# Optimization experiments

Measured on AMD Instinct MI355X. Metric: run time of the kernel, lower is better.

## Reference

```python
import jax, jax.numpy as jnp
import numpy as np

N = 100000        # nodes
E = 1600000       # edges (before self-loops)
F_IN = 128        # input feature dim
HID = 32          # hidden_channels
HEADS = 2
HC = HID * HEADS  # 64, per-conv output width (concat=True)
OUT = 40          # out_channels
NEG_SLOPE = 0.2   # PyG GATConv leaky_relu slope
BN_EPS = 1e-5


def setup_inputs() -> dict:
    key = jax.random.key(0)
    ks = jax.random.split(key, 16)
    g = lambda k, shape, s: jax.random.normal(k, shape, jnp.float32) * s
    node_feat = jax.random.normal(ks[0], (N, F_IN), jnp.float32)
    edge_index = jax.random.randint(ks[1], (2, E), 0, N, jnp.int32)
    inp = {
        "node_feat": node_feat,
        "edge_index": edge_index,
        "W1": g(ks[2], (F_IN, HC), 1.0 / np.sqrt(F_IN)),
        "a_src1": g(ks[3], (HEADS, HID), 0.1),
        "a_dst1": g(ks[4], (HEADS, HID), 0.1),
        "b1": jnp.zeros((HC,), jnp.float32),
        # BatchNorm1d(64) in eval mode (running stats)
        "bn_gamma": jnp.ones((HC,), jnp.float32),
        "bn_beta": jnp.zeros((HC,), jnp.float32),
        "bn_mean": g(ks[5], (HC,), 0.1),
        "bn_var": jax.random.uniform(ks[6], (HC,), jnp.float32, 0.5, 1.5),
        "W2": g(ks[7], (HC, HC), 1.0 / np.sqrt(HC)),
        "a_src2": g(ks[8], (HEADS, HID), 0.1),
        "a_dst2": g(ks[9], (HEADS, HID), 0.1),
        "b2": jnp.zeros((HC,), jnp.float32),
        # final projection 64 -> 40
        "Wf": g(ks[10], (HC, OUT), 1.0 / np.sqrt(HC)),
        "bf": jnp.zeros((OUT,), jnp.float32),
    }
    return inp


def _gat_layer(x, src, dst, W, a_s, a_d, b):
    # x: [N, Fin] -> h: [N, H, C]
    h = (x @ W).reshape(N, HEADS, HID)
    alpha_src = jnp.einsum('nhc,hc->nh', h, a_s)   # [N, H]
    alpha_dst = jnp.einsum('nhc,hc->nh', h, a_d)   # [N, H]
    e = jax.nn.leaky_relu(alpha_src[src] + alpha_dst[dst], NEG_SLOPE)  # [Etot, H]
    m = jax.lax.stop_gradient(jax.ops.segment_max(e, dst, num_segments=N))
    ex = jnp.exp(e - m[dst])
    denom = jax.ops.segment_sum(ex, dst, num_segments=N)
    alpha = ex / (denom[dst] + 1e-16)              # softmax over incoming edges
    msg = h[src] * alpha[:, :, None]               # [Etot, H, C]
    out = jax.ops.segment_sum(msg, dst, num_segments=N)  # [N, H, C]
    return out.reshape(N, HC) + b


def reference(node_feat, edge_index, W1, a_src1, a_dst1, b1,
              bn_gamma, bn_beta, bn_mean, bn_var,
              W2, a_src2, a_dst2, b2, Wf, bf):
    # add self-loops (PyG GATConv default add_self_loops=True)
    loop = jnp.arange(N, dtype=edge_index.dtype)
    src = jnp.concatenate([edge_index[0], loop])
    dst = jnp.concatenate([edge_index[1], loop])

    x1 = _gat_layer(node_feat, src, dst, W1, a_src1, a_dst1, b1)
    # BatchNorm1d eval + ELU (dropout is identity in eval)
    x1 = (x1 - bn_mean) * (bn_gamma / jnp.sqrt(bn_var + BN_EPS)) + bn_beta
    x1 = jax.nn.elu(x1)

    x2 = _gat_layer(x1, src, dst, W2, a_src2, a_dst2, b2)

    # JumpingKnowledge 'max': elementwise max over layer outputs
    xj = jnp.maximum(x1, x2)
    return xj @ Wf + bf
```

## Files before the change

kernel.cpp:

```cpp
#include <hip/hip_runtime.h>
#include <hip/hip_bf16.h>

#define N_NODES 100000
#define E_EDGES 1600000
#define ETOT    1700000
#define NB_SCAN 391
#define EQ4     400000
#define NB_EQ4  1563
#define EQ8     200000
#define NB_EQ8  782
#define NGB     1563
#define F_IN    128
#define HC      64
#define OUT_C   40
#define NEG_SLOPE 0.2f
#define BN_EPS  1e-5f

#define P_W1   0
#define P_AS1  8192
#define P_AD1  8256
#define P_B1   8320
#define P_BNG  8384
#define P_BNB  8448
#define P_BNM  8512
#define P_BNV  8576
#define P_W2   8640
#define P_AS2  12736
#define P_AD2  12800
#define P_B2   12864
#define P_WF   12928
#define P_BF   15488
#define P_TOT  15528

typedef __attribute__((ext_vector_type(8))) short short8;
typedef __attribute__((ext_vector_type(4))) float floatx4;
typedef __attribute__((ext_vector_type(4))) unsigned int uintx4;

__device__ __forceinline__ unsigned short f2bf(float f) {
    unsigned int u = __float_as_uint(f);
    unsigned int r = u + 0x7FFFu + ((u >> 16) & 1u);
    return (unsigned short)(r >> 16);
}

__device__ __forceinline__ float leaky(float v) { return v > 0.f ? v : NEG_SLOPE * v; }

__device__ __forceinline__ float red64(float v) {
#pragma unroll
    for (int off = 32; off > 0; off >>= 1) v += __shfl_xor(v, off, 64);
    return v;
}
__device__ __forceinline__ float red16(float v) {
#pragma unroll
    for (int off = 8; off > 0; off >>= 1) v += __shfl_xor(v, off, 64);
    return v;
}

__global__ __launch_bounds__(64) void detect_kernel(const unsigned short* __restrict__ x,
                                                    int* __restrict__ flag) {
    int t = threadIdx.x;
    bool huge = false;
#pragma unroll
    for (int i = 0; i < 4; ++i) {
        unsigned short u = x[(t * 4 + i) * 2];
        float v = __uint_as_float(((unsigned int)u) << 16);
        if (!(fabsf(v) < 1e4f)) huge = true;
    }
    unsigned long long b = __ballot(huge);
    if (t == 0) *flag = (b != 0ull) ? 1 : 0;
}

struct CvtArgs { const void* ptr[14]; int len[14]; };

__global__ __launch_bounds__(256) void cvt_params_kernel(CvtArgs a,
                                                         const int* __restrict__ flag,
                                                         float* __restrict__ dst) {
    int f = *flag;
    int i = blockIdx.x * 256 + threadIdx.x;
    if (i >= P_TOT) return;
    int k = 0, off = 0;
    while (i >= off + a.len[k]) { off += a.len[k]; ++k; }
    int j = i - off;
    float v = f ? ((const float*)a.ptr[k])[j]
                : __bfloat162float(((const __hip_bfloat16*)a.ptr[k])[j]);
    dst[i] = v;
}

__global__ __launch_bounds__(256) void build_frags_kernel(const float* __restrict__ prm,
                                                          unsigned short* __restrict__ fw1,
                                                          unsigned short* __restrict__ fw2) {
    int i = blockIdx.x * 256 + threadIdx.x;
    if (i < 8192) {
        int j = i & 7, l = (i >> 3) & 63, q = (i >> 9) & 3, t = i >> 11;
        int k = q * 32 + (l >> 4) * 8 + j;
        int n = t * 16 + (l & 15);
        fw1[i] = f2bf(prm[P_W1 + k * 64 + n]);
    } else if (i < 12288) {
        int f = i - 8192;
        int j = f & 7, l = (f >> 3) & 63, q = (f >> 9) & 1, t = f >> 10;
        int k = q * 32 + (l >> 4) * 8 + j;
        int n = t * 16 + (l & 15);
        fw2[f] = f2bf(prm[P_W2 + k * 64 + n]);
    }
}

__global__ __launch_bounds__(256) void fused_hist_gemm1_kernel(
        const int* __restrict__ ei, int* __restrict__ deg, int4* __restrict__ rank4,
        const void* __restrict__ x, const unsigned short* __restrict__ fw1,
        const float* __restrict__ prm, const int* __restrict__ flag,
        unsigned short* __restrict__ h_bf, float* __restrict__ as_,
        float* __restrict__ ad_) {
    __shared__ short lx[4 * 4 * 64 * 8];
    if (blockIdx.x < NB_EQ8) {
        int i8 = blockIdx.x * 256 + threadIdx.x;
        if (i8 >= EQ8) return;
        const unsigned long long* dst2 = (const unsigned long long*)(ei + E_EDGES);
        unsigned long long p0 = __builtin_nontemporal_load(&dst2[i8 * 4]);
        unsigned long long p1 = __builtin_nontemporal_load(&dst2[i8 * 4 + 1]);
        unsigned long long p2 = __builtin_nontemporal_load(&dst2[i8 * 4 + 2]);
        unsigned long long p3 = __builtin_nontemporal_load(&dst2[i8 * 4 + 3]);
        int d0 = (int)(p0 & 0xFFFFFFFFull), d1 = (int)(p0 >> 32);
        int d2 = (int)(p1 & 0xFFFFFFFFull), d3 = (int)(p1 >> 32);
        int d4 = (int)(p2 & 0xFFFFFFFFull), d5 = (int)(p2 >> 32);
        int d6 = (int)(p3 & 0xFFFFFFFFull), d7 = (int)(p3 >> 32);
        int r0 = atomicAdd(&deg[d0], 1);
        int r1 = atomicAdd(&deg[d1], 1);
        int r2 = atomicAdd(&deg[d2], 1);
        int r3 = atomicAdd(&deg[d3], 1);
        int r4 = atomicAdd(&deg[d4], 1);
        int r5 = atomicAdd(&deg[d5], 1);
        int r6 = atomicAdd(&deg[d6], 1);
        int r7 = atomicAdd(&deg[d7], 1);
        rank4[i8 * 2]     = make_int4(r0, r1, r2, r3);
        rank4[i8 * 2 + 1] = make_int4(r4, r5, r6, r7);
        return;
    }

    int t = threadIdx.x;
    int f = *flag;
    int base = (blockIdx.x - NB_EQ8) * 64;

#pragma unroll
    for (int i = 0; i < 4; ++i) {
        int cid = i * 256 + t;
        int m = cid >> 4, c = cid & 15;
        int q = c >> 2, g = c & 3;
        int loff = (((m >> 4) * 4 + q) * 64 + g * 16 + (m & 15)) * 8;
        int srow = base + m; if (srow > N_NODES - 1) srow = N_NODES - 1;
        short8 s;
        if (f) {
            const float4* p = (const float4*)((const float*)x + ((size_t)srow << 7) + (c << 3));
            float4 u0 = p[0], u1 = p[1];
            s[0] = (short)f2bf(u0.x); s[1] = (short)f2bf(u0.y);
            s[2] = (short)f2bf(u0.z); s[3] = (short)f2bf(u0.w);
            s[4] = (short)f2bf(u1.x); s[5] = (short)f2bf(u1.y);
            s[6] = (short)f2bf(u1.z); s[7] = (short)f2bf(u1.w);
        } else {
            s = *(const short8*)((const unsigned short*)x + ((size_t)srow << 7) + (c << 3));
        }
        *(short8*)&lx[loff] = s;
    }
    __syncthreads();

    int w = t >> 6, lane = t & 63;
    short8 a[4];
#pragma unroll
    for (int q = 0; q < 4; ++q) a[q] = *(short8*)&lx[((w * 4 + q) * 64 + lane) * 8];

    const short8* bw = (const short8*)fw1;
    floatx4 acc[4];
#pragma unroll
    for (int tt = 0; tt < 4; ++tt) acc[tt] = (floatx4){0.f, 0.f, 0.f, 0.f};
#pragma unroll
    for (int tt = 0; tt < 4; ++tt) {
#pragma unroll
        for (int q = 0; q < 4; ++q) {
            short8 b = bw[(tt * 4 + q) * 64 + lane];
            acc[tt] = __builtin_amdgcn_mfma_f32_16x16x32_bf16(a[q], b, acc[tt], 0, 0, 0);
        }
    }

    int cl = lane & 15, grp = lane >> 4;
#pragma unroll
    for (int tt = 0; tt < 4; ++tt) {
#pragma unroll
        for (int r = 0; r < 4; ++r) {
            int node = base + w * 16 + grp * 4 + r;
            if (node < N_NODES)
                h_bf[(size_t)node * 64 + tt * 16 + cl] = f2bf(acc[tt][r]);
        }
    }

    float as0 = prm[P_AS1 + 0  + cl], as1 = prm[P_AS1 + 16 + cl],
          as2 = prm[P_AS1 + 32 + cl], as3 = prm[P_AS1 + 48 + cl];
    float ad0 = prm[P_AD1 + 0  + cl], ad1 = prm[P_AD1 + 16 + cl],
          ad2 = prm[P_AD1 + 32 + cl], ad3 = prm[P_AD1 + 48 + cl];
#pragma unroll
    for (int r = 0; r < 4; ++r) {
        float sh0 = red16(acc[0][r] * as0 + acc[1][r] * as1);
        float sh1 = red16(acc[2][r] * as2 + acc[3][r] * as3);
        float dh0 = red16(acc[0][r] * ad0 + acc[1][r] * ad1);
        float dh1 = red16(acc[2][r] * ad2 + acc[3][r] * ad3);
        int node = base + w * 16 + grp * 4 + r;
        if (cl == 0 && node < N_NODES) {
            as_[node * 2] = sh0;  as_[node * 2 + 1] = sh1;
            ad_[node * 2] = dh0;  ad_[node * 2 + 1] = dh1;
        }
    }
}

__global__ __launch_bounds__(256) void scanA_kernel(const int* __restrict__ deg,
                                                    int* __restrict__ bsum) {
    __shared__ int sm[256];
    int t = threadIdx.x;
    int i = blockIdx.x * 256 + t;
    sm[t] = (i < N_NODES) ? deg[i] + 1 : 0;
    __syncthreads();
    for (int off = 128; off > 0; off >>= 1) {
        if (t < off) sm[t] += sm[t + off];
        __syncthreads();
    }
    if (t == 0) bsum[blockIdx.x] = sm[0];
}

__global__ __launch_bounds__(512) void scanB_kernel(const int* __restrict__ bsum,
                                                    int* __restrict__ boff,
                                                    int* __restrict__ row_start) {
    __shared__ int sm[512];
    int t = threadIdx.x;
    int v = (t < NB_SCAN) ? bsum[t] : 0;
    sm[t] = v;
    __syncthreads();
    for (int off = 1; off < 512; off <<= 1) {
        int o = (t >= off) ? sm[t - off] : 0;
        __syncthreads();
        sm[t] += o;
        __syncthreads();
    }
    if (t < NB_SCAN) boff[t] = sm[t] - v;
    if (t == NB_SCAN - 1) row_start[N_NODES] = sm[t];
}

__global__ __launch_bounds__(256) void scanC_kernel(const int* __restrict__ deg,
                                                    const int* __restrict__ boff,
                                                    int* __restrict__ row_start,
                                                    int* __restrict__ col) {
    __shared__ int sm[256];
    int t = threadIdx.x;
    int i = blockIdx.x * 256 + t;
    int v = (i < N_NODES) ? deg[i] + 1 : 0;
    sm[t] = v;
    __syncthreads();
    for (int off = 1; off < 256; off <<= 1) {
        int o = (t >= off) ? sm[t - off] : 0;
        __syncthreads();
        sm[t] += o;
        __syncthreads();
    }
    if (i < N_NODES) {
        int excl = sm[t] - v + boff[blockIdx.x];
        row_start[i] = excl;
        col[excl]    = i;
    }
}

__global__ __launch_bounds__(256) void scatter_kernel(const int* __restrict__ ei,
                                                      const int4* __restrict__ rank4,
                                                      const int* __restrict__ row_start,
                                                      int* __restrict__ col) {
    int i4 = blockIdx.x * 256 + threadIdx.x;
    if (i4 >= EQ4) return;
    const unsigned long long* dst2 = (const unsigned long long*)(ei + E_EDGES);
    const unsigned long long* src2 = (const unsigned long long*)ei;
    unsigned long long p0 = __builtin_nontemporal_load(&dst2[i4 * 2]);
    unsigned long long p1 = __builtin_nontemporal_load(&dst2[i4 * 2 + 1]);
    unsigned long long q0 = __builtin_nontemporal_load(&src2[i4 * 2]);
    unsigned long long q1 = __builtin_nontemporal_load(&src2[i4 * 2 + 1]);
    int4 r = rank4[i4];
    int d0 = (int)(p0 & 0xFFFFFFFFull), d1 = (int)(p0 >> 32);
    int d2 = (int)(p1 & 0xFFFFFFFFull), d3 = (int)(p1 >> 32);
    int s0 = (int)(q0 & 0xFFFFFFFFull), s1 = (int)(q0 >> 32);
    int s2 = (int)(q1 & 0xFFFFFFFFull), s3 = (int)(q1 >> 32);
    int b0 = row_start[d0];
    int b1 = row_start[d1];
    int b2 = row_start[d2];
    int b3 = row_start[d3];
    col[b0 + 1 + r.x] = s0;
    col[b1 + 1 + r.y] = s1;
    col[b2 + 1 + r.z] = s2;
    col[b3 + 1 + r.w] = s3;
}

__global__ __launch_bounds__(128) void gemm2_kernel(const unsigned short* __restrict__ x1_bf,
                                                    const unsigned short* __restrict__ fw2,
                                                    const float* __restrict__ prm,
                                                    unsigned short* __restrict__ h_bf,
                                                    float* __restrict__ as_,
                                                    float* __restrict__ ad_) {
    __shared__ short lx[2 * 2 * 64 * 8];
    int t = threadIdx.x;
    int base = blockIdx.x * 32;

#pragma unroll
    for (int i = 0; i < 2; ++i) {
        int cid = i * 128 + t;
        int m = cid >> 3, c = cid & 7;
        int q = c >> 2, g = c & 3;
        int loff = (((m >> 4) * 2 + q) * 64 + g * 16 + (m & 15)) * 8;
        short8 s = *(const short8*)(x1_bf + ((size_t)(base + m) << 6) + (c << 3));
        *(short8*)&lx[loff] = s;
    }
    __syncthreads();

    int w = t >> 6, lane = t & 63;
    short8 a[2];
#pragma unroll
    for (int q = 0; q < 2; ++q) a[q] = *(short8*)&lx[((w * 2 + q) * 64 + lane) * 8];

    const short8* bw = (const short8*)fw2;
    floatx4 acc[4];
#pragma unroll
    for (int tt = 0; tt < 4; ++tt) acc[tt] = (floatx4){0.f, 0.f, 0.f, 0.f};
#pragma unroll
    for (int tt = 0; tt < 4; ++tt) {
#pragma unroll
        for (int q = 0; q < 2; ++q) {
            short8 b = bw[(tt * 2 + q) * 64 + lane];
            acc[tt] = __builtin_amdgcn_mfma_f32_16x16x32_bf16(a[q], b, acc[tt], 0, 0, 0);
        }
    }

    int cl = lane & 15, grp = lane >> 4;
#pragma unroll
    for (int tt = 0; tt < 4; ++tt) {
#pragma unroll
        for (int r = 0; r < 4; ++r) {
            int node = base + w * 16 + grp * 4 + r;
            h_bf[(size_t)node * 64 + tt * 16 + cl] = f2bf(acc[tt][r]);
        }
    }

    float as0 = prm[P_AS2 + 0  + cl], as1 = prm[P_AS2 + 16 + cl],
          as2 = prm[P_AS2 + 32 + cl], as3 = prm[P_AS2 + 48 + cl];
    float ad0 = prm[P_AD2 + 0  + cl], ad1 = prm[P_AD2 + 16 + cl],
          ad2 = prm[P_AD2 + 32 + cl], ad3 = prm[P_AD2 + 48 + cl];
#pragma unroll
    for (int r = 0; r < 4; ++r) {
        float sh0 = red16(acc[0][r] * as0 + acc[1][r] * as1);
        float sh1 = red16(acc[2][r] * as2 + acc[3][r] * as3);
        float dh0 = red16(acc[0][r] * ad0 + acc[1][r] * ad1);
        float dh1 = red16(acc[2][r] * ad2 + acc[3][r] * ad3);
        if (cl == 0) {
            int node = base + w * 16 + grp * 4 + r;
            as_[node * 2] = sh0;  as_[node * 2 + 1] = sh1;
            ad_[node * 2] = dh0;  ad_[node * 2 + 1] = dh1;
        }
    }
}

__device__ __forceinline__ float slot_reduce(float acc[8], int lane) {
    int slot = lane & 7;
    bool b2 = (slot & 4) != 0;
#pragma unroll
    for (int q = 0; q < 4; ++q) {
        float send = b2 ? acc[q] : acc[q + 4];
        float recv = __shfl_xor(send, 4, 64);
        acc[q] = (b2 ? acc[q + 4] : acc[q]) + recv;
    }
    bool b1 = (slot & 2) != 0;
#pragma unroll
    for (int q = 0; q < 2; ++q) {
        float send = b1 ? acc[q] : acc[q + 2];
        float recv = __shfl_xor(send, 2, 64);
        acc[q] = (b1 ? acc[q + 2] : acc[q]) + recv;
    }
    bool b0 = (slot & 1) != 0;
    float send = b0 ? acc[0] : acc[1];
    float recv = __shfl_xor(send, 1, 64);
    return (b0 ? acc[1] : acc[0]) + recv;
}

template<int NK>
__device__ __forceinline__ void agg_rounds(const unsigned short* __restrict__ hb,
                                           const float* __restrict__ as_,
                                           const int* __restrict__ col,
                                           int rs, int koff, int last,
                                           int slot, int hi, float advh,
                                           float acc[8], float& sw) {
    int ce[NK]; float av[NK]; uintx4 dv[NK];
#pragma unroll
    for (int k = 0; k < NK; ++k) {
        int e = rs + koff + k * 8 + slot;
        ce[k] = col[e < last ? e : last];
    }
#pragma unroll
    for (int k = 0; k < NK; ++k)
        dv[k] = *(const uintx4*)(hb + ((size_t)ce[k] << 6));
#pragma unroll
    for (int k = 0; k < NK; ++k)
        av[k] = as_[ce[k] * 2 + hi];

    if constexpr (NK == 1) {
        asm volatile("" : "+v"(dv[0]), "+v"(av[0]));
    } else if constexpr (NK == 2) {
        asm volatile("" : "+v"(dv[0]), "+v"(dv[1]), "+v"(av[0]), "+v"(av[1]));
    } else if constexpr (NK == 3) {
        asm volatile("" : "+v"(dv[0]), "+v"(dv[1]), "+v"(dv[2]),
                          "+v"(av[0]), "+v"(av[1]), "+v"(av[2]));
    } else {
        asm volatile("" : "+v"(dv[0]), "+v"(dv[1]), "+v"(dv[2]), "+v"(dv[3]),
                          "+v"(av[0]), "+v"(av[1]), "+v"(av[2]), "+v"(av[3]));
    }

#pragma unroll
    for (int k = 0; k < NK; ++k) {
        int e = rs + koff + k * 8 + slot;
        float w = (e <= last) ? __expf(leaky(av[k] + advh)) : 0.f;
        sw += w;
#pragma unroll
        for (int q = 0; q < 4; ++q) {
            unsigned int dw = dv[k][q];
            acc[2 * q]     = fmaf(w, __uint_as_float(dw << 16),         acc[2 * q]);
            acc[2 * q + 1] = fmaf(w, __uint_as_float(dw & 0xFFFF0000u), acc[2 * q + 1]);
        }
    }
}

__device__ __forceinline__ float agg_core(const unsigned short* __restrict__ h_bf,
                                          const float* __restrict__ as_,
                                          const float* __restrict__ ad_,
                                          const int* __restrict__ col,
                                          int v, int rs, int re, int lane) {
    int deg  = re - rs;
    int slot = lane & 7;
    int cg   = lane >> 3;
    int hi   = cg >> 2;
    if (deg <= 64) {
        float advh = ad_[v * 2 + hi];
        const unsigned short* hb = h_bf + (cg << 3);
        int last = re - 1;
        float acc[8] = {0.f,0.f,0.f,0.f,0.f,0.f,0.f,0.f};
        float sw = 0.f;

        if (deg <= 8) {
            agg_rounds<1>(hb, as_, col, rs, 0, last, slot, hi, advh, acc, sw);
        } else if (deg <= 16) {
            agg_rounds<2>(hb, as_, col, rs, 0, last, slot, hi, advh, acc, sw);
        } else if (deg <= 24) {
            agg_rounds<3>(hb, as_, col, rs, 0, last, slot, hi, advh, acc, sw);
        } else {
            agg_rounds<4>(hb, as_, col, rs, 0, last, slot, hi, advh, acc, sw);
            if (deg > 32)
                agg_rounds<4>(hb, as_, col, rs, 32, last, slot, hi, advh, acc, sw);
        }

        sw += __shfl_xor(sw, 1, 64);
        sw += __shfl_xor(sw, 2, 64);
        sw += __shfl_xor(sw, 4, 64);
        float rdh = 1.f / (sw + 1e-16f);

        return slot_reduce(acc, lane) * rdh;
    } else {
        int head = lane >> 5;
        float adv0 = ad_[v * 2], adv1 = ad_[v * 2 + 1];
        float advh = head ? adv1 : adv0;
        float s0 = 0.f, s1 = 0.f;
        for (int e = rs + lane; e < re; e += 64) {
            int s = col[e];
            float2 av = *(const float2*)&as_[s * 2];
            s0 += __expf(leaky(av.x + adv0));
            s1 += __expf(leaky(av.y + adv1));
        }
        s0 = red64(s0); s1 = red64(s1);
        float rdh = 1.f / ((head ? s1 : s0) + 1e-16f);
        float a0 = 0.f;
        for (int e = rs; e < re; ++e) {
            int s = col[e];
            float w = __expf(leaky(as_[s * 2 + head] + advh));
            unsigned short u = h_bf[(size_t)s * 64 + lane];
            a0 = fmaf(w, __uint_as_float(((unsigned int)u) << 16), a0);
        }
        return a0 * rdh;
    }
}

__global__ __launch_bounds__(256, 6) void agg1_kernel(const unsigned short* __restrict__ h_bf,
                                                   const float* __restrict__ as_,
                                                   const float* __restrict__ ad_,
                                                   const int* __restrict__ row_start,
                                                   const int* __restrict__ col,
                                                   const float* __restrict__ bias,
                                                   const float* __restrict__ bn_g,
                                                   const float* __restrict__ bn_b,
                                                   const float* __restrict__ bn_m,
                                                   const float* __restrict__ bn_v,
                                                   unsigned short* __restrict__ x1_bf) {
    int t = threadIdx.x, wid = t >> 6, lane = t & 63;
    int v = blockIdx.x * 4 + wid;
    int rs = row_start[v], re = row_start[v + 1];
    float acc = agg_core(h_bf, as_, ad_, col, v, rs, re, lane);
    float r = acc + bias[lane];
    float scale = bn_g[lane] * rsqrtf(bn_v[lane] + BN_EPS);
    r = (r - bn_m[lane]) * scale + bn_b[lane];
    r = r > 0.f ? r : expm1f(r);
    x1_bf[(size_t)v * 64 + lane] = f2bf(r);
}

__global__ __launch_bounds__(256, 6) void agg2_kernel(const unsigned short* __restrict__ h_bf,
                                                   const float* __restrict__ as_,
                                                   const float* __restrict__ ad_,
                                                   const int* __restrict__ row_start,
                                                   const int* __restrict__ col,
                                                   const float* __restrict__ prm,
                                                   const unsigned short* __restrict__ x1_bf,
                                                   const int* __restrict__ flag,
                                                   void* __restrict__ out) {
    __shared__ float Wfs[2560];
    __shared__ float xsh[4][64];
    int t = threadIdx.x;
#pragma unroll
    for (int i = 0; i < 10; ++i) Wfs[i * 256 + t] = prm[P_WF + i * 256 + t];

    int wid = t >> 6, lane = t & 63;
    int v = blockIdx.x * 4 + wid;
    int rs = row_start[v], re = row_start[v + 1];
    float acc = agg_core(h_bf, as_, ad_, col, v, rs, re, lane);
    float x2 = acc + prm[P_B2 + lane];
    unsigned short u = x1_bf[(size_t)v * 64 + lane];
    float x1v = __uint_as_float(((unsigned int)u) << 16);
    xsh[wid][lane] = fmaxf(x1v, x2);
    __syncthreads();

    if (t < 160) {
        int n = t / 40, o = t - n * 40;
        float po = 0.f;
#pragma unroll
        for (int c = 0; c < 64; c += 4) {
            po = fmaf(xsh[n][c],     Wfs[c * 40 + o],       po);
            po = fmaf(xsh[n][c + 1], Wfs[(c + 1) * 40 + o], po);
            po = fmaf(xsh[n][c + 2], Wfs[(c + 2) * 40 + o], po);
            po = fmaf(xsh[n][c + 3], Wfs[(c + 3) * 40 + o], po);
        }
        float r = po + prm[P_BF + o];
        size_t idx = (size_t)(blockIdx.x * 4 + n) * 40 + o;
        if (*flag) ((float*)out)[idx] = r;
        else ((__hip_bfloat16*)out)[idx] = __float2bfloat16(r);
    }
}

extern "C" void kernel_launch(void* const* d_in, const int* in_sizes, int n_in,
                              void* d_out, int out_size, void* d_ws, size_t ws_size,
                              hipStream_t stream) {
    (void)in_sizes; (void)n_in; (void)out_size; (void)ws_size;
    const void* node_feat = d_in[0];
    const int*  edge_idx  = (const int*)d_in[1];

    char* ws = (char*)d_ws;
    size_t off = 0;
    auto alloc = [&](size_t bytes) -> void* {
        void* p = ws + off;
        off += (bytes + 255) & ~(size_t)255;
        return p;
    };
    unsigned short* h_bf  = (unsigned short*)alloc((size_t)N_NODES * 64 * 2);
    unsigned short* x1_bf = (unsigned short*)alloc((size_t)N_NODES * 64 * 2);
    float* as_ = (float*)alloc((size_t)N_NODES * 2 * 4);
    float* ad_ = (float*)alloc((size_t)N_NODES * 2 * 4);
    int* deg       = (int*)alloc((size_t)N_NODES * 4);
    int* row_start = (int*)alloc((size_t)(N_NODES + 1) * 4);
    int4* rank4    = (int4*)alloc((size_t)EQ4 * 16);
    int* col       = (int*)alloc((size_t)ETOT * 4);
    int* bsum      = (int*)alloc((size_t)NB_SCAN * 4);
    int* boff      = (int*)alloc((size_t)NB_SCAN * 4);
    float* prm     = (float*)alloc((size_t)P_TOT * 4);
    unsigned short* fw1 = (unsigned short*)alloc(8192 * 2);
    unsigned short* fw2 = (unsigned short*)alloc(4096 * 2);
    int* flag      = (int*)alloc(256);

    detect_kernel<<<1, 64, 0, stream>>>((const unsigned short*)node_feat, flag);
    CvtArgs ca;
    const int lens[14] = {8192, 64, 64, 64, 64, 64, 64, 64, 4096, 64, 64, 64, 2560, 40};
    for (int i = 0; i < 14; ++i) { ca.ptr[i] = d_in[i + 2]; ca.len[i] = lens[i]; }
    cvt_params_kernel<<<(P_TOT + 255) / 256, 256, 0, stream>>>(ca, flag, prm);
    build_frags_kernel<<<48, 256, 0, stream>>>(prm, fw1, fw2);

    hipMemsetAsync(deg, 0, (size_t)N_NODES * 4, stream);
    fused_hist_gemm1_kernel<<<NB_EQ8 + NGB, 256, 0, stream>>>(
        edge_idx, deg, rank4, node_feat, fw1, prm, flag, h_bf, as_, ad_);
    scanA_kernel<<<NB_SCAN, 256, 0, stream>>>(deg, bsum);
    scanB_kernel<<<1, 512, 0, stream>>>(bsum, boff, row_start);
    scanC_kernel<<<NB_SCAN, 256, 0, stream>>>(deg, boff, row_start, col);
    scatter_kernel<<<NB_EQ4, 256, 0, stream>>>(edge_idx, rank4, row_start, col);

    agg1_kernel<<<N_NODES / 4, 256, 0, stream>>>(h_bf, as_, ad_, row_start, col,
                                                 prm + P_B1, prm + P_BNG, prm + P_BNB,
                                                 prm + P_BNM, prm + P_BNV, x1_bf);
    gemm2_kernel<<<N_NODES / 32, 128, 0, stream>>>(x1_bf, fw2, prm,
                                                   h_bf, as_, ad_);
    agg2_kernel<<<N_NODES / 4, 256, 0, stream>>>(h_bf, as_, ad_, row_start, col,
                                                 prm, x1_bf, flag, d_out);
}
```

Baseline: 367.0 us.

## Build CSR via two-level bucket sort instead of per-node global atomics

Replaces the per-destination global atomic histogram, three-pass scan and rank-based scatter with a bucketed counting sort over 196 buckets of 512 nodes. Block-local LDS histograms reduce global atomics, edges are staged into an intermediate buffer grouped by bucket, and a per-bucket kernel builds row_start and col with LDS atomics and a local scan. This targets the cost of random global atomics and scattered writes, but adds an extra 8-byte-per-edge staging write and read, and the final CSR kernel uses only 196 blocks, so it may leave the GPU underutilized.

```diff
diff --git a/kernel.cpp b/kernel.cpp
--- a/kernel.cpp
+++ b/kernel.cpp
@@ -4,12 +4,10 @@
 #define N_NODES 100000
 #define E_EDGES 1600000
 #define ETOT    1700000
-#define NB_SCAN 391
-#define EQ4     400000
-#define NB_EQ4  1563
 #define EQ8     200000
 #define NB_EQ8  782
 #define NGB     1563
+#define NBUK    196
 #define F_IN    128
 #define HC      64
 #define OUT_C   40
@@ -103,39 +101,45 @@
     }
 }
 
+
 __global__ __launch_bounds__(256) void fused_hist_gemm1_kernel(
-        const int* __restrict__ ei, int* __restrict__ deg, int4* __restrict__ rank4,
+        const int* __restrict__ ei, int* __restrict__ bkt_cnt,
         const void* __restrict__ x, const unsigned short* __restrict__ fw1,
         const float* __restrict__ prm, const int* __restrict__ flag,
         unsigned short* __restrict__ h_bf, float* __restrict__ as_,
         float* __restrict__ ad_) {
     __shared__ short lx[4 * 4 * 64 * 8];
+    int t = threadIdx.x;
     if (blockIdx.x < NB_EQ8) {
-        int i8 = blockIdx.x * 256 + threadIdx.x;
-        if (i8 >= EQ8) return;
-        const unsigned long long* dst2 = (const unsigned long long*)(ei + E_EDGES);
-        unsigned long long p0 = __builtin_nontemporal_load(&dst2[i8 * 4]);
-        unsigned long long p1 = __builtin_nontemporal_load(&dst2[i8 * 4 + 1]);
-        unsigned long long p2 = __builtin_nontemporal_load(&dst2[i8 * 4 + 2]);
-        unsigned long long p3 = __builtin_nontemporal_load(&dst2[i8 * 4 + 3]);
-        int d0 = (int)(p0 & 0xFFFFFFFFull), d1 = (int)(p0 >> 32);
-        int d2 = (int)(p1 & 0xFFFFFFFFull), d3 = (int)(p1 >> 32);
-        int d4 = (int)(p2 & 0xFFFFFFFFull), d5 = (int)(p2 >> 32);
-        int d6 = (int)(p3 & 0xFFFFFFFFull), d7 = (int)(p3 >> 32);
-        int r0 = atomicAdd(&deg[d0], 1);
-        int r1 = atomicAdd(&deg[d1], 1);
-        int r2 = atomicAdd(&deg[d2], 1);
-        int r3 = atomicAdd(&deg[d3], 1);
-        int r4 = atomicAdd(&deg[d4], 1);
-        int r5 = atomicAdd(&deg[d5], 1);
-        int r6 = atomicAdd(&deg[d6], 1);
-        int r7 = atomicAdd(&deg[d7], 1);
-        rank4[i8 * 2]     = make_int4(r0, r1, r2, r3);
-        rank4[i8 * 2 + 1] = make_int4(r4, r5, r6, r7);
+        int* cnt = (int*)lx;
+        if (t < NBUK) cnt[t] = 0;
+        __syncthreads();
+        int i8 = blockIdx.x * 256 + t;
+        if (i8 < EQ8) {
+            const unsigned long long* dst2 = (const unsigned long long*)(ei + E_EDGES);
+            unsigned long long p0 = __builtin_nontemporal_load(&dst2[i8 * 4]);
+            unsigned long long p1 = __builtin_nontemporal_load(&dst2[i8 * 4 + 1]);
+            unsigned long long p2 = __builtin_nontemporal_load(&dst2[i8 * 4 + 2]);
+            unsigned long long p3 = __builtin_nontemporal_load(&dst2[i8 * 4 + 3]);
+            atomicAdd(&cnt[(int)(p0 & 0xFFFFFFFFull) >> 9], 1);
+            atomicAdd(&cnt[(int)(p0 >> 32) >> 9], 1);
+            atomicAdd(&cnt[(int)(p1 & 0xFFFFFFFFull) >> 9], 1);
+            atomicAdd(&cnt[(int)(p1 >> 32) >> 9], 1);
+            atomicAdd(&cnt[(int)(p2 & 0xFFFFFFFFull) >> 9], 1);
+            atomicAdd(&cnt[(int)(p2 >> 32) >> 9], 1);
+            atomicAdd(&cnt[(int)(p3 & 0xFFFFFFFFull) >> 9], 1);
+            atomicAdd(&cnt[(int)(p3 >> 32) >> 9], 1);
+        }
+        __syncthreads();
+        if (t < NBUK) {
+            int tb = t + (int)(blockIdx.x % NBUK);
+            tb -= (tb >= NBUK) ? NBUK : 0;
+            int c = cnt[tb];
+            if (c) atomicAdd(&bkt_cnt[tb], c);
+        }
         return;
     }
 
-    int t = threadIdx.x;
     int f = *flag;
     int base = (blockIdx.x - NB_EQ8) * 64;
 
@@ -208,46 +212,13 @@
     }
 }
 
-__global__ __launch_bounds__(256) void scanA_kernel(const int* __restrict__ deg,
-                                                    int* __restrict__ bsum) {
+__global__ __launch_bounds__(256) void bucket_scan_kernel(const int* __restrict__ bkt_cnt,
+                                                          int* __restrict__ boff,
+                                                          int* __restrict__ bcur,
+                                                          int* __restrict__ row_start) {
     __shared__ int sm[256];
     int t = threadIdx.x;
-    int i = blockIdx.x * 256 + t;
-    sm[t] = (i < N_NODES) ? deg[i] + 1 : 0;
-    __syncthreads();
-    for (int off = 128; off > 0; off >>= 1) {
-        if (t < off) sm[t] += sm[t + off];
-        __syncthreads();
-    }
-    if (t == 0) bsum[blockIdx.x] = sm[0];
-}
-
-__global__ __launch_bounds__(512) void scanB_kernel(const int* __restrict__ bsum,
-                                                    int* __restrict__ boff,
-                                                    int* __restrict__ row_start) {
-    __shared__ int sm[512];
-    int t = threadIdx.x;
-    int v = (t < NB_SCAN) ? bsum[t] : 0;
-    sm[t] = v;
-    __syncthreads();
-    for (int off = 1; off < 512; off <<= 1) {
-        int o = (t >= off) ? sm[t - off] : 0;
-        __syncthreads();
-        sm[t] += o;
-        __syncthreads();
-    }
-    if (t < NB_SCAN) boff[t] = sm[t] - v;
-    if (t == NB_SCAN - 1) row_start[N_NODES] = sm[t];
-}
-
-__global__ __launch_bounds__(256) void scanC_kernel(const int* __restrict__ deg,
-                                                    const int* __restrict__ boff,
-                                                    int* __restrict__ row_start,
-                                                    int* __restrict__ col) {
-    __shared__ int sm[256];
-    int t = threadIdx.x;
-    int i = blockIdx.x * 256 + t;
-    int v = (i < N_NODES) ? deg[i] + 1 : 0;
+    int v = (t < NBUK) ? bkt_cnt[t] : 0;
     sm[t] = v;
     __syncthreads();
     for (int off = 1; off < 256; off <<= 1) {
@@ -256,38 +227,108 @@
         sm[t] += o;
         __syncthreads();
     }
-    if (i < N_NODES) {
-        int excl = sm[t] - v + boff[blockIdx.x];
-        row_start[i] = excl;
-        col[excl]    = i;
-    }
-}
-
-__global__ __launch_bounds__(256) void scatter_kernel(const int* __restrict__ ei,
-                                                      const int4* __restrict__ rank4,
-                                                      const int* __restrict__ row_start,
-                                                      int* __restrict__ col) {
-    int i4 = blockIdx.x * 256 + threadIdx.x;
-    if (i4 >= EQ4) return;
-    const unsigned long long* dst2 = (const unsigned long long*)(ei + E_EDGES);
-    const unsigned long long* src2 = (const unsigned long long*)ei;
-    unsigned long long p0 = __builtin_nontemporal_load(&dst2[i4 * 2]);
-    unsigned long long p1 = __builtin_nontemporal_load(&dst2[i4 * 2 + 1]);
-    unsigned long long q0 = __builtin_nontemporal_load(&src2[i4 * 2]);
-    unsigned long long q1 = __builtin_nontemporal_load(&src2[i4 * 2 + 1]);
-    int4 r = rank4[i4];
-    int d0 = (int)(p0 & 0xFFFFFFFFull), d1 = (int)(p0 >> 32);
-    int d2 = (int)(p1 & 0xFFFFFFFFull), d3 = (int)(p1 >> 32);
-    int s0 = (int)(q0 & 0xFFFFFFFFull), s1 = (int)(q0 >> 32);
-    int s2 = (int)(q1 & 0xFFFFFFFFull), s3 = (int)(q1 >> 32);
-    int b0 = row_start[d0];
-    int b1 = row_start[d1];
-    int b2 = row_start[d2];
-    int b3 = row_start[d3];
-    col[b0 + 1 + r.x] = s0;
-    col[b1 + 1 + r.y] = s1;
-    col[b2 + 1 + r.z] = s2;
-    col[b3 + 1 + r.w] = s3;
+    if (t < NBUK) { int e = sm[t] - v; boff[t] = e; bcur[t] = e; }
+    if (t == NBUK - 1) boff[NBUK] = sm[t];
+    if (t == 0) row_start[N_NODES] = ETOT;
+}
+
+__global__ __launch_bounds__(256) void bucket_scatter_kernel(const int* __restrict__ ei,
+                                                             int* __restrict__ bcur,
+                                                             unsigned long long* __restrict__ estage) {
+    __shared__ int cnt[NBUK];
+    __shared__ int base[NBUK];
+    int t = threadIdx.x;
+    if (t < NBUK) cnt[t] = 0;
+    __syncthreads();
+    int i8 = blockIdx.x * 256 + t;
+    bool valid = i8 < EQ8;
+    int d[8], s[8], rl[8];
+    if (valid) {
+        const unsigned long long* dst2 = (const unsigned long long*)(ei + E_EDGES);
+        const unsigned long long* src2 = (const unsigned long long*)ei;
+        unsigned long long p0 = __builtin_nontemporal_load(&dst2[i8 * 4]);
+        unsigned long long p1 = __builtin_nontemporal_load(&dst2[i8 * 4 + 1]);
+        unsigned long long p2 = __builtin_nontemporal_load(&dst2[i8 * 4 + 2]);
+        unsigned long long p3 = __builtin_nontemporal_load(&dst2[i8 * 4 + 3]);
+        unsigned long long q0 = __builtin_nontemporal_load(&src2[i8 * 4]);
+        unsigned long long q1 = __builtin_nontemporal_load(&src2[i8 * 4 + 1]);
+        unsigned long long q2 = __builtin_nontemporal_load(&src2[i8 * 4 + 2]);
+        unsigned long long q3 = __builtin_nontemporal_load(&src2[i8 * 4 + 3]);
+        d[0] = (int)(p0 & 0xFFFFFFFFull); d[1] = (int)(p0 >> 32);
+        d[2] = (int)(p1 & 0xFFFFFFFFull); d[3] = (int)(p1 >> 32);
+        d[4] = (int)(p2 & 0xFFFFFFFFull); d[5] = (int)(p2 >> 32);
+        d[6] = (int)(p3 & 0xFFFFFFFFull); d[7] = (int)(p3 >> 32);
+        s[0] = (int)(q0 & 0xFFFFFFFFull); s[1] = (int)(q0 >> 32);
+        s[2] = (int)(q1 & 0xFFFFFFFFull); s[3] = (int)(q1 >> 32);
+        s[4] = (int)(q2 & 0xFFFFFFFFull); s[5] = (int)(q2 >> 32);
+        s[6] = (int)(q3 & 0xFFFFFFFFull); s[7] = (int)(q3 >> 32);
+#pragma unroll
+        for (int k = 0; k < 8; ++k) rl[k] = atomicAdd(&cnt[d[k] >> 9], 1);
+    }
+    __syncthreads();
+    if (t < NBUK) {
+        int tb = t + (int)(blockIdx.x % NBUK);
+        tb -= (tb >= NBUK) ? NBUK : 0;
+        int c = cnt[tb];
+        base[tb] = c ? atomicAdd(&bcur[tb], c) : 0;
+    }
+    __syncthreads();
+    if (valid) {
+#pragma unroll
+        for (int k = 0; k < 8; ++k) {
+            int buk = d[k] >> 9;
+            estage[base[buk] + rl[k]] =
+                (unsigned long long)(unsigned int)s[k] |
+                ((unsigned long long)(unsigned int)d[k] << 32);
+        }
+    }
+}
+
+__global__ __launch_bounds__(256) void bucket_csr_kernel(const unsigned long long* __restrict__ estage,
+                                                         const int* __restrict__ boff,
+                                                         int* __restrict__ row_start,
+                                                         int* __restrict__ col) {
+    __shared__ int ldeg[512];
+    __shared__ int sA[512], sB[512];
+    __shared__ int exq[512];
+    int b = blockIdx.x, t = threadIdx.x;
+    int nbase = b << 9;
+    int nb = N_NODES - nbase; if (nb > 512) nb = 512;
+    int e0 = boff[b], e1 = boff[b + 1];
+    int rb = e0 + nbase;
+    ldeg[t] = 0; ldeg[t + 256] = 0;
+    __syncthreads();
+    for (int e = e0 + t; e < e1; e += 256) {
+        int dl = (int)(estage[e] >> 32) - nbase;
+        atomicAdd(&ldeg[dl], 1);
+    }
+    __syncthreads();
+    int v0 = (t < nb) ? ldeg[t] + 1 : 0;
+    int v1 = (t + 256 < nb) ? ldeg[t + 256] + 1 : 0;
+    sA[t] = v0; sA[t + 256] = v1;
+    __syncthreads();
+    int* A = sA; int* Bp = sB;
+    for (int off = 1; off < 512; off <<= 1) {
+        int a0 = A[t] + ((t >= off) ? A[t - off] : 0);
+        int a1 = A[t + 256] + ((t + 256 >= off) ? A[t + 256 - off] : 0);
+        Bp[t] = a0; Bp[t + 256] = a1;
+        __syncthreads();
+        int* tmp = A; A = Bp; Bp = tmp;
+    }
+    exq[t] = A[t] - v0;
+    exq[t + 256] = A[t + 256] - v1;
+    __syncthreads();
+    if (t < nb) { int rsv = rb + exq[t]; row_start[nbase + t] = rsv; col[rsv] = nbase + t; }
+    if (t + 256 < nb) { int rsv = rb + exq[t + 256]; row_start[nbase + t + 256] = rsv; col[rsv] = nbase + t + 256; }
+    ldeg[t] = 0; ldeg[t + 256] = 0;
+    __syncthreads();
+    for (int e = e0 + t; e < e1; e += 256) {
+        unsigned long long p = estage[e];
+        int s = (int)(p & 0xFFFFFFFFull);
+        int dl = (int)(p >> 32) - nbase;
+        int r = atomicAdd(&ldeg[dl], 1);
+        col[rb + exq[dl] + 1 + r] = s;
+    }
 }
 
 __global__ __launch_bounds__(128) void gemm2_kernel(const unsigned short* __restrict__ x1_bf,
@@ -565,12 +606,12 @@
     unsigned short* x1_bf = (unsigned short*)alloc((size_t)N_NODES * 64 * 2);
     float* as_ = (float*)alloc((size_t)N_NODES * 2 * 4);
     float* ad_ = (float*)alloc((size_t)N_NODES * 2 * 4);
-    int* deg       = (int*)alloc((size_t)N_NODES * 4);
     int* row_start = (int*)alloc((size_t)(N_NODES + 1) * 4);
-    int4* rank4    = (int4*)alloc((size_t)EQ4 * 16);
+    unsigned long long* estage = (unsigned long long*)alloc((size_t)E_EDGES * 8);
     int* col       = (int*)alloc((size_t)ETOT * 4);
-    int* bsum      = (int*)alloc((size_t)NB_SCAN * 4);
-    int* boff      = (int*)alloc((size_t)NB_SCAN * 4);
+    int* bkt_cnt   = (int*)alloc((size_t)NBUK * 4);
+    int* bkt_off   = (int*)alloc((size_t)(NBUK + 1) * 4);
+    int* bkt_cur   = (int*)alloc((size_t)NBUK * 4);
     float* prm     = (float*)alloc((size_t)P_TOT * 4);
     unsigned short* fw1 = (unsigned short*)alloc(8192 * 2);
     unsigned short* fw2 = (unsigned short*)alloc(4096 * 2);
@@ -583,13 +624,12 @@
     cvt_params_kernel<<<(P_TOT + 255) / 256, 256, 0, stream>>>(ca, flag, prm);
     build_frags_kernel<<<48, 256, 0, stream>>>(prm, fw1, fw2);
 
-    hipMemsetAsync(deg, 0, (size_t)N_NODES * 4, stream);
+    hipMemsetAsync(bkt_cnt, 0, (size_t)NBUK * 4, stream);
     fused_hist_gemm1_kernel<<<NB_EQ8 + NGB, 256, 0, stream>>>(
-        edge_idx, deg, rank4, node_feat, fw1, prm, flag, h_bf, as_, ad_);
-    scanA_kernel<<<NB_SCAN, 256, 0, stream>>>(deg, bsum);
-    scanB_kernel<<<1, 512, 0, stream>>>(bsum, boff, row_start);
-    scanC_kernel<<<NB_SCAN, 256, 0, stream>>>(deg, boff, row_start, col);
-    scatter_kernel<<<NB_EQ4, 256, 0, stream>>>(edge_idx, rank4, row_start, col);
+        edge_idx, bkt_cnt, node_feat, fw1, prm, flag, h_bf, as_, ad_);
+    bucket_scan_kernel<<<1, 256, 0, stream>>>(bkt_cnt, bkt_off, bkt_cur, row_start);
+    bucket_scatter_kernel<<<NB_EQ8, 256, 0, stream>>>(edge_idx, bkt_cur, estage);
+    bucket_csr_kernel<<<NBUK, 256, 0, stream>>>(estage, bkt_off, row_start, col);
 
     agg1_kernel<<<N_NODES / 4, 256, 0, stream>>>(h_bf, as_, ad_, row_start, col,
                                                  prm + P_B1, prm + P_BNG, prm + P_BNB,
```

Measured after the change: 333.7 us. -9.1%, faster.
